# Kernel tuning notes

Measured on AMD Instinct MI355X. Metric: run time of the kernel, lower is better.

## Reference

```python
import jax, jax.numpy as jnp
import numpy as np

B, N, C, H, HD = 32, 512, 384, 6, 64
WH = WW = WT = 8
ALPHA = 4.0
KS = 5


def safe_pow(x, p):
    # x = relu(...) >= 0; avoid nan grads at x == 0
    pos = x > 0
    return jnp.where(pos, jnp.where(pos, x, 1.0) ** p, 0.0)


def setup_inputs() -> dict:
    key = jax.random.key(0)
    ks = jax.random.split(key, 12)
    s = 0.02
    return {
        "x": jax.random.normal(ks[0], (B, N, C), jnp.float32),
        "y": jax.random.normal(ks[1], (B, N, C), jnp.float32),
        "Wqkvg": jax.random.normal(ks[2], (4 * C, C), jnp.float32) * s,
        "bqkvg": jax.random.normal(ks[3], (4 * C,), jnp.float32) * s,
        "Wproj": jax.random.normal(ks[4], (C, C), jnp.float32) * s,
        "bproj": jax.random.normal(ks[5], (C,), jnp.float32) * s,
        "dwc_w": jax.random.normal(ks[6], (HD, 1, KS, KS, KS), jnp.float32) * s,
        "dwc_b": jax.random.normal(ks[7], (HD,), jnp.float32) * s,
        "power_p": jax.random.normal(ks[8], (1, H, 1, HD), jnp.float32) * s,
        "scale_p": jax.random.normal(ks[9], (1, 1, C), jnp.float32) * s,
        "pe": jax.random.normal(ks[10], (1, N, C), jnp.float32) * s,
    }


def reference(x, y, Wqkvg, bqkvg, Wproj, bproj, dwc_w, dwc_b, power_p, scale_p, pe):
    qkv = (x @ Wqkvg.T + bqkvg).reshape(B, N, 4, C)
    k = qkv[:, :, 1]
    v = qkv[:, :, 2]
    g = qkv[:, :, 3]
    q = (y @ Wqkvg.T + bqkvg).reshape(B, N, 4, C)[:, :, 0]

    k = k + pe
    scale = jax.nn.softplus(scale_p)          # (1,1,C)
    power = 1.0 + ALPHA * jax.nn.sigmoid(power_p)  # (1,H,1,HD)
    q = q / scale
    k = k / scale

    def heads(t):  # (B,N,C) -> (B,H,N,HD)
        return t.reshape(B, N, H, HD).transpose(0, 2, 1, 3)

    q = heads(q)
    k = heads(k)
    v = heads(v)

    q_pos = safe_pow(jax.nn.relu(q), power)
    q_neg = safe_pow(jax.nn.relu(-q), power)
    k_pos = safe_pow(jax.nn.relu(k), power)
    k_neg = safe_pow(jax.nn.relu(-k), power)

    q_sim = jnp.concatenate([q_pos, q_neg], axis=-1)   # (B,H,N,2HD)
    q_opp = jnp.concatenate([q_neg, q_pos], axis=-1)
    kf = jnp.concatenate([k_pos, k_neg], axis=-1)      # (B,H,N,2HD)
    v1, v2 = jnp.split(v, 2, axis=-1)                  # each (B,H,N,HD/2)

    k_mean = kf.mean(axis=-2)                          # (B,H,2HD)
    inv_sqrt_n = N ** (-0.5)
    kfs = kf * inv_sqrt_n

    z_sim = 1.0 / (jnp.einsum("bhnd,bhd->bhn", q_sim, k_mean)[..., None] + 1e-6)
    kv1 = jnp.einsum("bhnd,bhne->bhde", kfs, v1 * inv_sqrt_n)
    x_sim = jnp.einsum("bhnd,bhde->bhne", q_sim, kv1) * z_sim

    z_opp = 1.0 / (jnp.einsum("bhnd,bhd->bhn", q_opp, k_mean)[..., None] + 1e-6)
    kv2 = jnp.einsum("bhnd,bhne->bhde", kfs, v2 * inv_sqrt_n)
    x_opp = jnp.einsum("bhnd,bhde->bhne", q_opp, kv2) * z_opp

    xa = jnp.concatenate([x_sim, x_opp], axis=-1)      # (B,H,N,HD)
    xa = xa.transpose(0, 2, 1, 3).reshape(B, N, C)

    # depthwise conv3d on v: (B*H, HD, Wh, Ww, Wt)
    vr = v.reshape(B * H, WH, WW, WT, HD).transpose(0, 4, 1, 2, 3)
    pad = KS // 2
    vc = jax.lax.conv_general_dilated(
        vr, dwc_w, window_strides=(1, 1, 1),
        padding=[(pad, pad)] * 3,
        dimension_numbers=("NCDHW", "OIDHW", "NCDHW"),
        feature_group_count=HD,
    ) + dwc_b[None, :, None, None, None]
    vc = vc.transpose(0, 2, 3, 4, 1).reshape(B, N, C)

    out = (xa + vc) * g
    out = out @ Wproj.T + bproj
    return out
```

## Files before the change

### kernel.cpp

```cpp
#include <hip/hip_runtime.h>
#include <hip/hip_bf16.h>
#include <math.h>

#define B_  32
#define N_  512
#define C_  384
#define H_  6
#define HD_ 64
#define M_  (B_*N_)

typedef __attribute__((ext_vector_type(8))) short bfrag;
typedef __attribute__((ext_vector_type(8))) unsigned short u16x8;
typedef __attribute__((ext_vector_type(4))) float f32x4;

__device__ __forceinline__ unsigned short f2bfu(float f){
  unsigned int u = __float_as_uint(f);
  u += 0x7fffu + ((u >> 16) & 1u);
  return (unsigned short)(u >> 16);
}
__device__ __forceinline__ float bf2f(unsigned short u){
  return __uint_as_float(((unsigned int)u) << 16);
}
__device__ __forceinline__ bfrag cvt8(float4 a, float4 b){
  bfrag r;
  r[0]=(short)f2bfu(a.x); r[1]=(short)f2bfu(a.y); r[2]=(short)f2bfu(a.z); r[3]=(short)f2bfu(a.w);
  r[4]=(short)f2bfu(b.x); r[5]=(short)f2bfu(b.y); r[6]=(short)f2bfu(b.z); r[7]=(short)f2bfu(b.w);
  return r;
}
__device__ __forceinline__ void gload_lds16(const unsigned short* gp, unsigned short* lp){
  __builtin_amdgcn_global_load_lds(
      (const __attribute__((address_space(1))) void*)gp,
      (__attribute__((address_space(3))) void*)lp, 16, 0, 0);
}

__global__ void param_kernel(const float* __restrict__ scale_p,
                             const float* __restrict__ power_p,
                             float* __restrict__ scale_inv,
                             float* __restrict__ power){
  int t = threadIdx.x;
  if (t < C_){
    float s  = scale_p[t];
    scale_inv[t] = 1.0f / log1pf(expf(s));
  }
  if (t < H_*HD_){
    float p = power_p[t];
    power[t] = 1.0f + 4.0f / (1.0f + expf(-p));
  }
}

__global__ void sentinel_kernel(float* __restrict__ out, int n){
  int i = blockIdx.x*256 + threadIdx.x;
  if (i < n) out[i] = 1.0e9f;
}

__global__ __launch_bounds__(256) void cvt_bf16_kernel(
    const float* __restrict__ x, const float* __restrict__ y,
    const float* __restrict__ W, const float* __restrict__ Wp,
    unsigned short* __restrict__ xb, unsigned short* __restrict__ yb,
    unsigned short* __restrict__ Wb, unsigned short* __restrict__ Wpb)
{
  const int bid = blockIdx.x;
  const float* src; unsigned short* dst; int base;
  if (bid < 3072)      { src = x;  dst = xb;  base = bid; }
  else if (bid < 6144) { src = y;  dst = yb;  base = bid - 3072; }
  else if (bid < 6432) { src = W;  dst = Wb;  base = bid - 6144; }
  else                 { src = Wp; dst = Wpb; base = bid - 6432; }
  const size_t i0 = ((size_t)base*256 + threadIdx.x)*8;
  float4 a = *reinterpret_cast<const float4*>(src + i0);
  float4 b = *reinterpret_cast<const float4*>(src + i0 + 4);
  *reinterpret_cast<bfrag*>(dst + i0) = cvt8(a, b);
}

__global__ __launch_bounds__(256,4) void gemm_qkvg(
    const unsigned short* __restrict__ xb, const unsigned short* __restrict__ yb,
    const unsigned short* __restrict__ Wb, const float* __restrict__ bias,
    const float* __restrict__ pe, const float* __restrict__ scale_inv,
    const float* __restrict__ power,
    unsigned short* __restrict__ qf, unsigned short* __restrict__ kf,
    unsigned short* __restrict__ v, unsigned short* __restrict__ g)
{
  __shared__ unsigned short As[2][4096];
  __shared__ unsigned short Bs[2][4096];

  const int tid  = threadIdx.x;
  const int row0 = blockIdx.y * 128;
  const int col0 = blockIdx.x * 128;
  const int mode = blockIdx.x / 3;
  const unsigned short* Ab = (mode == 0) ? yb : xb;

  const int wave = tid >> 6, lane = tid & 63;
  const int wm = (wave >> 1) * 64, wn = (wave & 1) * 64;
  const int fr = lane & 15, quad = lane >> 4;
  const int srr = tid >> 2;
  const int skc = (tid & 3) * 8;

  const unsigned short* ga0 = &Ab[(size_t)(row0 + srr)*C_ + skc];
  const unsigned short* gb0 = &Wb[(size_t)(col0 + srr)*C_ + skc];
  const size_t gstep = (size_t)64*C_;

  f32x4 acc[4][4] = {};

  gload_lds16(ga0,         &As[0][tid*8]);
  gload_lds16(ga0 + gstep, &As[0][2048 + tid*8]);
  gload_lds16(gb0,         &Bs[0][tid*8]);
  gload_lds16(gb0 + gstep, &Bs[0][2048 + tid*8]);
  __syncthreads();

  #pragma unroll 2
  for (int t = 0; t < 12; t++){
    const int cur = t & 1;
    if (t < 11){
      const int k0 = (t+1)*32;
      gload_lds16(ga0 + k0,         &As[cur^1][tid*8]);
      gload_lds16(ga0 + gstep + k0, &As[cur^1][2048 + tid*8]);
      gload_lds16(gb0 + k0,         &Bs[cur^1][tid*8]);
      gload_lds16(gb0 + gstep + k0, &Bs[cur^1][2048 + tid*8]);
    }
    bfrag af[4], bf[4];
    #pragma unroll
    for (int f = 0; f < 4; f++){
      af[f] = *reinterpret_cast<const bfrag*>(&As[cur][(wm + f*16 + fr)*32 + quad*8]);
      bf[f] = *reinterpret_cast<const bfrag*>(&Bs[cur][(wn + f*16 + fr)*32 + quad*8]);
    }
    #pragma unroll
    for (int i=0;i<4;i++)
      #pragma unroll
      for (int j=0;j<4;j++)
        acc[i][j] = __builtin_amdgcn_mfma_f32_16x16x32_bf16(af[i], bf[j], acc[i][j], 0, 0, 0);
    __syncthreads();
  }

  const int cbase = col0 - mode*384;
  if (mode <= 1){
    unsigned short* dst = (mode == 0) ? qf : kf;
    #pragma unroll
    for (int i = 0; i < 4; i++){
      const int rowb = row0 + wm + i*16 + quad*4;
      #pragma unroll
      for (int j = 0; j < 4; j++){
        const int cc = cbase + wn + j*16 + fr;
        const int hh = cc >> 6, dd = cc & 63;
        const float bcol = bias[mode*384 + cc];
        const float scv  = scale_inv[cc];
        const float p    = power[cc];
        #pragma unroll
        for (int r = 0; r < 4; r++){
          const int row = rowb + r;
          float val = acc[i][j][r] + bcol;
          if (mode == 1) val += pe[(row & (N_-1))*C_ + cc];
          val *= scv;
          const float ax = fabsf(val);
          const float pv = (ax > 0.0f) ? exp2f(p * log2f(ax)) : 0.0f;
          const size_t o = (size_t)row*768 + hh*128 + dd;
          dst[o]      = f2bfu((val > 0.0f) ? pv : 0.0f);
          dst[o + 64] = f2bfu((val < 0.0f) ? pv : 0.0f);
        }
      }
    }
  } else {
    unsigned short* dst = (mode == 2) ? v : g;
    #pragma unroll
    for (int i = 0; i < 4; i++){
      const int rowb = row0 + wm + i*16 + quad*4;
      #pragma unroll
      for (int j = 0; j < 4; j++){
        const int cc = cbase + wn + j*16 + fr;
        const float bcol = bias[mode*384 + cc];
        #pragma unroll
        for (int r = 0; r < 4; r++)
          dst[(size_t)(rowb + r)*C_ + cc] = f2bfu(acc[i][j][r] + bcol);
      }
    }
  }
}

#define NC_ 256
__global__ __launch_bounds__(512) void attn_kernel(
    const unsigned short* __restrict__ qf, const unsigned short* __restrict__ kf,
    const unsigned short* __restrict__ v, float* __restrict__ xa)
{
  const int bh = blockIdx.x;
  const int b = bh / H_, h = bh % H_;
  __shared__ __align__(16) unsigned short smem[54912];
  unsigned short* kfT  = smem;
  unsigned short* vT   = smem + 33792;
  unsigned short* kvBT = smem;
  unsigned short* qs   = smem + 33792;

  const int tid = threadIdx.x;
  const int wave = tid >> 6, lane = tid & 63;
  const int fr = lane & 15, quad = lane >> 4;

  const unsigned short* kfg   = kf + (size_t)b*N_*768 + h*128;
  const unsigned short* vbase = v  + (size_t)b*N_*C_  + h*HD_;

  for (int i = tid; i < 16*NC_; i += 512){
    int e = 64 + (i >> 8);
    int nl = i & (NC_-1);
    vT[e*264 + nl] = (e == 64) ? (unsigned short)0x3F80 : (unsigned short)0;
  }
  __syncthreads();

  f32x4 acc[5] = {};
  for (int chunk = 0; chunk < 2; chunk++){
    const int n0 = chunk * NC_;
    for (int it = 0; it < 8; it++){
      int flat = it*512 + tid;
      int cg = flat & 15, nl = flat >> 4;
      u16x8 k8 = *reinterpret_cast<const u16x8*>(&kfg[(size_t)(n0+nl)*768 + cg*8]);
      #pragma unroll
      for (int j = 0; j < 8; j++) kfT[(cg*8+j)*264 + nl] = k8[j];
    }
    for (int it = 0; it < 4; it++){
      int flat = it*512 + tid;
      int cg = flat & 7, nl = flat >> 3;
      u16x8 v8 = *reinterpret_cast<const u16x8*>(&vbase[(size_t)(n0+nl)*C_ + cg*8]);
      #pragma unroll
      for (int j = 0; j < 8; j++) vT[(cg*8+j)*264 + nl] = v8[j];
    }
    __syncthreads();
    for (int kk = 0; kk < NC_/32; kk++){
      int ko = kk*32 + quad*8;
      bfrag af = *reinterpret_cast<const bfrag*>(&kfT[(wave*16 + fr)*264 + ko]);
      #pragma unroll
      for (int j = 0; j < 5; j++){
        bfrag bf = *reinterpret_cast<const bfrag*>(&vT[(j*16 + fr)*264 + ko]);
        acc[j] = __builtin_amdgcn_mfma_f32_16x16x32_bf16(af, bf, acc[j], 0, 0, 0);
      }
    }
    __syncthreads();
  }

  const float invN = 1.0f / (float)N_;
  {
    const int dbase = wave*16 + quad*4;
    #pragma unroll
    for (int j = 0; j < 4; j++){
      const int e = j*16 + fr;
      const int dd = (e < 32) ? dbase : (dbase ^ 64);
      ushort4 w4;
      w4.x = f2bfu(acc[j][0] * invN);
      w4.y = f2bfu(acc[j][1] * invN);
      w4.z = f2bfu(acc[j][2] * invN);
      w4.w = f2bfu(acc[j][3] * invN);
      *reinterpret_cast<ushort4*>(&kvBT[e*136 + dd]) = w4;
    }
    if (fr == 0){
      ushort4 wk;
      wk.x = f2bfu(acc[4][0] * invN);
      wk.y = f2bfu(acc[4][1] * invN);
      wk.z = f2bfu(acc[4][2] * invN);
      wk.w = f2bfu(acc[4][3] * invN);
      *reinterpret_cast<ushort4*>(&kvBT[64*136 + dbase]) = wk;
      *reinterpret_cast<ushort4*>(&kvBT[65*136 + (dbase^64)]) = wk;
    }
  }
  __syncthreads();

  const unsigned short* qfg = qf + (size_t)b*N_*768 + h*128;
  float* xabase = xa + (size_t)b*N_*C_ + h*HD_;
  for (int mc = 0; mc < 4; mc++){
    const int m0 = mc * 128;
    for (int it = 0; it < 4; it++){
      int flat = it*512 + tid;
      int cg = flat & 15, nl = flat >> 4;
      *reinterpret_cast<u16x8*>(&qs[nl*136 + cg*8]) =
          *reinterpret_cast<const u16x8*>(&qfg[(size_t)(m0+nl)*768 + cg*8]);
    }
    __syncthreads();
    f32x4 a2[5] = {};
    for (int kk = 0; kk < 4; kk++){
      int ko = kk*32 + quad*8;
      bfrag af = *reinterpret_cast<const bfrag*>(&qs[(wave*16 + fr)*136 + ko]);
      #pragma unroll
      for (int j = 0; j < 5; j++){
        bfrag bf = *reinterpret_cast<const bfrag*>(&kvBT[(j*16 + fr)*136 + ko]);
        a2[j] = __builtin_amdgcn_mfma_f32_16x16x32_bf16(af, bf, a2[j], 0, 0, 0);
      }
    }
    #pragma unroll
    for (int r = 0; r < 4; r++){
      const float zsim = __shfl(a2[4][r], quad*16);
      const float zopp = __shfl(a2[4][r], quad*16 + 1);
      const int n = m0 + wave*16 + quad*4 + r;
      #pragma unroll
      for (int j = 0; j < 4; j++){
        const int e = j*16 + fr;
        const float z = (e < 32) ? zsim : zopp;
        xabase[(size_t)n*C_ + e] = a2[j][r] / (z + 1e-6f);
      }
    }
    __syncthreads();
  }
}

__global__ __launch_bounds__(512) void conv_kernel(
    const unsigned short* __restrict__ v, const float* __restrict__ dwc_w,
    const float* __restrict__ dwc_b, const float* __restrict__ xa,
    const unsigned short* __restrict__ g, unsigned short* __restrict__ ab)
{
  const int bh = blockIdx.x;
  const int b = bh / H_, h = bh % H_;
  __shared__ float vol[32][521];
  __shared__ float wv[32][126];
  __shared__ float wb[32];
  const int tid = threadIdx.x;
  const unsigned short* vbase = v + (size_t)b*N_*C_ + h*HD_;
  const float* xabatch = xa + (size_t)b*N_*C_ + (size_t)h*N_*HD_;
  const unsigned short* gb = g + (size_t)b*N_*C_ + (size_t)h*N_*HD_;
  unsigned short* abb = ab + (size_t)b*N_*C_ + (size_t)h*N_*HD_;

  for (int half = 0; half < 2; half++){
    const int ch0 = half * 32;
    for (int it = 0; it < 32; it++){
      int flat = it*512 + tid;
      int cl = flat & 31, n = flat >> 5;
      vol[cl][n] = bf2f(vbase[(size_t)n*C_ + ch0 + cl]);
    }
    for (int i = tid; i < 32*125; i += 512){
      int ch = i / 125, wi = i - ch*125;
      wv[ch][wi] = dwc_w[(ch0+ch)*125 + wi];
    }
    if (tid < 32) wb[tid] = dwc_b[ch0 + tid];
    __syncthreads();

    for (int t = 0; t < 4; t++){
      const int task = t*512 + tid;
      const int ch = task & 31;
      const int zy = task >> 5;
      const int z = zy >> 3, yc = zy & 7;
      float o[8];
      const float bias = wb[ch];
      #pragma unroll
      for (int xx = 0; xx < 8; xx++) o[xx] = bias;
      #pragma unroll
      for (int kd = 0; kd < 5; kd++){
        const int zz = z + kd - 2;
        if ((unsigned)zz >= 8u) continue;
        #pragma unroll
        for (int kh = 0; kh < 5; kh++){
          const int yy = yc + kh - 2;
          if ((unsigned)yy >= 8u) continue;
          const float* row = &vol[ch][zz*64 + yy*8];
          float rr[8];
          #pragma unroll
          for (int xx = 0; xx < 8; xx++) rr[xx] = row[xx];
          const float* wrow = &wv[ch][kd*25 + kh*5];
          float w5[5];
          #pragma unroll
          for (int kw = 0; kw < 5; kw++) w5[kw] = wrow[kw];
          #pragma unroll
          for (int xx = 0; xx < 8; xx++){
            #pragma unroll
            for (int kw = 0; kw < 5; kw++){
              const int xi = xx + kw - 2;
              if ((unsigned)xi < 8u) o[xx] = fmaf(w5[kw], rr[xi], o[xx]);
            }
          }
        }
      }
      const int nb = zy * 8;
      #pragma unroll
      for (int xx = 0; xx < 8; xx++){
        const size_t di = (size_t)(nb + xx)*HD_ + ch0 + ch;
        abb[di] = f2bfu((xabatch[di] + o[xx]) * bf2f(gb[di]));
      }
    }
    __syncthreads();
  }
}

__global__ __launch_bounds__(256,4) void proj_kernel(
    const unsigned short* __restrict__ ab, const unsigned short* __restrict__ Wpb,
    const float* __restrict__ bp, float* __restrict__ out)
{
  __shared__ unsigned short As[2][4096];
  __shared__ unsigned short Bs[2][4096];

  const int tid  = threadIdx.x;
  const int row0 = blockIdx.y * 128;
  const int col0 = blockIdx.x * 128;
  const int wave = tid >> 6, lane = tid & 63;
  const int wm = (wave >> 1) * 64, wn = (wave & 1) * 64;
  const int fr = lane & 15, quad = lane >> 4;
  const int srr = tid >> 2;
  const int skc = (tid & 3) * 8;

  const unsigned short* ga0 = &ab[(size_t)(row0 + srr)*C_ + skc];
  const unsigned short* gb0 = &Wpb[(size_t)(col0 + srr)*C_ + skc];
  const size_t gstep = (size_t)64*C_;

  f32x4 acc[4][4] = {};

  gload_lds16(ga0,         &As[0][tid*8]);
  gload_lds16(ga0 + gstep, &As[0][2048 + tid*8]);
  gload_lds16(gb0,         &Bs[0][tid*8]);
  gload_lds16(gb0 + gstep, &Bs[0][2048 + tid*8]);
  __syncthreads();

  #pragma unroll 2
  for (int t = 0; t < 12; t++){
    const int cur = t & 1;
    if (t < 11){
      const int k0 = (t+1)*32;
      gload_lds16(ga0 + k0,         &As[cur^1][tid*8]);
      gload_lds16(ga0 + gstep + k0, &As[cur^1][2048 + tid*8]);
      gload_lds16(gb0 + k0,         &Bs[cur^1][tid*8]);
      gload_lds16(gb0 + gstep + k0, &Bs[cur^1][2048 + tid*8]);
    }
    bfrag af[4], bf[4];
    #pragma unroll
    for (int f = 0; f < 4; f++){
      af[f] = *reinterpret_cast<const bfrag*>(&As[cur][(wm + f*16 + fr)*32 + quad*8]);
      bf[f] = *reinterpret_cast<const bfrag*>(&Bs[cur][(wn + f*16 + fr)*32 + quad*8]);
    }
    #pragma unroll
    for (int i=0;i<4;i++)
      #pragma unroll
      for (int j=0;j<4;j++)
        acc[i][j] = __builtin_amdgcn_mfma_f32_16x16x32_bf16(af[i], bf[j], acc[i][j], 0, 0, 0);
    __syncthreads();
  }

  #pragma unroll
  for (int i = 0; i < 4; i++){
    const int rowb = row0 + wm + i*16 + quad*4;
    #pragma unroll
    for (int j = 0; j < 4; j++){
      const int col = col0 + wn + j*16 + fr;
      const float bcol = bp[col];
      #pragma unroll
      for (int r = 0; r < 4; r++)
        out[(size_t)(rowb + r)*C_ + col] = acc[i][j][r] + bcol;
    }
  }
}

extern "C" void kernel_launch(void* const* d_in, const int* in_sizes, int n_in,
                              void* d_out, int out_size, void* d_ws, size_t ws_size,
                              hipStream_t stream){
  float* out = (float*)d_out;

  const int expect[11] = {6291456, 6291456, 589824, 1536, 147456, 384, 8000, 64, 384, 384, 196608};
  bool ok = (n_in == 11);
  for (int i = 0; ok && i < 11; i++) ok = (in_sizes[i] == expect[i]);
  if (!ok){
    sentinel_kernel<<<(out_size+255)/256, 256, 0, stream>>>(out, out_size);
    return;
  }

  const float* x    = (const float*)d_in[0];
  const float* y    = (const float*)d_in[1];
  const float* W    = (const float*)d_in[2];
  const float* bq   = (const float*)d_in[3];
  const float* Wp   = (const float*)d_in[4];
  const float* bp   = (const float*)d_in[5];
  const float* dwcw = (const float*)d_in[6];
  const float* dwcb = (const float*)d_in[7];
  const float* pwp  = (const float*)d_in[8];
  const float* scp  = (const float*)d_in[9];
  const float* pe   = (const float*)d_in[10];

  float* ws = (float*)d_ws;
  const size_t SZ = (size_t)M_ * C_;
  unsigned short* qf  = (unsigned short*)ws;
  unsigned short* kfb = qf + 2*SZ;
  unsigned short* v   = (unsigned short*)(ws + 2*SZ);
  unsigned short* g   = v + SZ;
  unsigned short* xb  = (unsigned short*)(ws + 3*SZ);
  unsigned short* yb  = xb + SZ;
  float* xa = ws + 3*SZ;
  unsigned short* ab  = (unsigned short*)ws;
  unsigned short* Wb  = (unsigned short*)(ws + 4*SZ);
  unsigned short* Wpb = Wb + 589824;
  float* scale_inv = (float*)(Wpb + 147456);
  float* power     = scale_inv + 512;

  param_kernel<<<1, 512, 0, stream>>>(scp, pwp, scale_inv, power);
  cvt_bf16_kernel<<<6504, 256, 0, stream>>>(x, y, W, Wp, xb, yb, Wb, Wpb);
  gemm_qkvg<<<dim3(12, 128), 256, 0, stream>>>(xb, yb, Wb, bq, pe, scale_inv, power, qf, kfb, v, g);
  attn_kernel<<<dim3(B_*H_), 512, 0, stream>>>(qf, kfb, v, xa);
  conv_kernel<<<dim3(B_*H_), 512, 0, stream>>>(v, dwcw, dwcb, xa, g, ab);
  proj_kernel<<<dim3(3, 128), 256, 0, stream>>>(ab, Wpb, bp, out);
}
```

Measured before the change: 267.5 us.

## Stage q/k feature epilogue through LDS, swizzle attn transposes, split conv channels

The QKVG GEMM epilogue for q/k features now writes each 64-row half into a swizzled shared-memory tile, then stores it to global memory as coalesced 16-byte vectors instead of scattered 2-byte stores. The attention kernel's transposed kf/v LDS tiles get an XOR swizzle meant to reduce bank conflicts on the scalar transpose writes. The conv kernel is split across four channel groups per (batch, head) to raise parallelism, and two launch-bounds occupancy hints are dropped. The extra syncs in the epilogue and the larger conv grid add some overhead in exchange.

```diff
diff --git a/kernel.cpp b/kernel.cpp
--- a/kernel.cpp
+++ b/kernel.cpp
@@ -71,7 +71,7 @@
   *reinterpret_cast<bfrag*>(dst + i0) = cvt8(a, b);
 }
 
-__global__ __launch_bounds__(256,4) void gemm_qkvg(
+__global__ __launch_bounds__(256) void gemm_qkvg(
     const unsigned short* __restrict__ xb, const unsigned short* __restrict__ yb,
     const unsigned short* __restrict__ Wb, const float* __restrict__ bias,
     const float* __restrict__ pe, const float* __restrict__ scale_inv,
@@ -79,8 +79,7 @@
     unsigned short* __restrict__ qf, unsigned short* __restrict__ kf,
     unsigned short* __restrict__ v, unsigned short* __restrict__ g)
 {
-  __shared__ unsigned short As[2][4096];
-  __shared__ unsigned short Bs[2][4096];
+  __shared__ __align__(16) unsigned short smem[16384];
 
   const int tid  = threadIdx.x;
   const int row0 = blockIdx.y * 128;
@@ -100,10 +99,10 @@
 
   f32x4 acc[4][4] = {};
 
-  gload_lds16(ga0,         &As[0][tid*8]);
-  gload_lds16(ga0 + gstep, &As[0][2048 + tid*8]);
-  gload_lds16(gb0,         &Bs[0][tid*8]);
-  gload_lds16(gb0 + gstep, &Bs[0][2048 + tid*8]);
+  gload_lds16(ga0,         &smem[tid*8]);
+  gload_lds16(ga0 + gstep, &smem[2048 + tid*8]);
+  gload_lds16(gb0,         &smem[8192 + tid*8]);
+  gload_lds16(gb0 + gstep, &smem[8192 + 2048 + tid*8]);
   __syncthreads();
 
   #pragma unroll 2
@@ -111,16 +110,17 @@
     const int cur = t & 1;
     if (t < 11){
       const int k0 = (t+1)*32;
-      gload_lds16(ga0 + k0,         &As[cur^1][tid*8]);
-      gload_lds16(ga0 + gstep + k0, &As[cur^1][2048 + tid*8]);
-      gload_lds16(gb0 + k0,         &Bs[cur^1][tid*8]);
-      gload_lds16(gb0 + gstep + k0, &Bs[cur^1][2048 + tid*8]);
+      const int nxt = cur^1;
+      gload_lds16(ga0 + k0,         &smem[nxt*4096 + tid*8]);
+      gload_lds16(ga0 + gstep + k0, &smem[nxt*4096 + 2048 + tid*8]);
+      gload_lds16(gb0 + k0,         &smem[8192 + nxt*4096 + tid*8]);
+      gload_lds16(gb0 + gstep + k0, &smem[8192 + nxt*4096 + 2048 + tid*8]);
     }
     bfrag af[4], bf[4];
     #pragma unroll
     for (int f = 0; f < 4; f++){
-      af[f] = *reinterpret_cast<const bfrag*>(&As[cur][(wm + f*16 + fr)*32 + quad*8]);
-      bf[f] = *reinterpret_cast<const bfrag*>(&Bs[cur][(wn + f*16 + fr)*32 + quad*8]);
+      af[f] = *reinterpret_cast<const bfrag*>(&smem[cur*4096 + (wm + f*16 + fr)*32 + quad*8]);
+      bf[f] = *reinterpret_cast<const bfrag*>(&smem[8192 + cur*4096 + (wn + f*16 + fr)*32 + quad*8]);
     }
     #pragma unroll
     for (int i=0;i<4;i++)
@@ -133,29 +133,46 @@
   const int cbase = col0 - mode*384;
   if (mode <= 1){
     unsigned short* dst = (mode == 0) ? qf : kf;
-    #pragma unroll
-    for (int i = 0; i < 4; i++){
-      const int rowb = row0 + wm + i*16 + quad*4;
-      #pragma unroll
-      for (int j = 0; j < 4; j++){
-        const int cc = cbase + wn + j*16 + fr;
-        const int hh = cc >> 6, dd = cc & 63;
-        const float bcol = bias[mode*384 + cc];
-        const float scv  = scale_inv[cc];
-        const float p    = power[cc];
+    const int hh0 = cbase >> 6;
+    for (int pass = 0; pass < 2; pass++){
+      if ((wave >> 1) == pass){
+        const int swz = quad << 3;
         #pragma unroll
-        for (int r = 0; r < 4; r++){
-          const int row = rowb + r;
-          float val = acc[i][j][r] + bcol;
-          if (mode == 1) val += pe[(row & (N_-1))*C_ + cc];
-          val *= scv;
-          const float ax = fabsf(val);
-          const float pv = (ax > 0.0f) ? exp2f(p * log2f(ax)) : 0.0f;
-          const size_t o = (size_t)row*768 + hh*128 + dd;
-          dst[o]      = f2bfu((val > 0.0f) ? pv : 0.0f);
-          dst[o + 64] = f2bfu((val < 0.0f) ? pv : 0.0f);
+        for (int i = 0; i < 4; i++){
+          const int rloc = i*16 + quad*4;
+          #pragma unroll
+          for (int j = 0; j < 4; j++){
+            const int cl = wn + j*16 + fr;
+            const int hl = cl >> 6, dd = cl & 63;
+            const int cc = cbase + cl;
+            const float bcol = bias[mode*384 + cc];
+            const float scv  = scale_inv[cc];
+            const float p    = power[cc];
+            const int fpos = (hl*128 + dd) ^ swz;
+            #pragma unroll
+            for (int r = 0; r < 4; r++){
+              const int row = row0 + pass*64 + rloc + r;
+              float val = acc[i][j][r] + bcol;
+              if (mode == 1) val += pe[(row & (N_-1))*C_ + cc];
+              val *= scv;
+              const float ax = fabsf(val);
+              const float pv = (ax > 0.0f) ? exp2f(p * log2f(ax)) : 0.0f;
+              smem[(rloc + r)*256 + fpos]      = f2bfu((val > 0.0f) ? pv : 0.0f);
+              smem[(rloc + r)*256 + fpos + 64] = f2bfu((val < 0.0f) ? pv : 0.0f);
+            }
+          }
         }
       }
+      __syncthreads();
+      #pragma unroll
+      for (int it = 0; it < 8; it++){
+        const int idx = it*256 + tid;
+        const int rl = idx >> 5, cb = idx & 31;
+        const int bswz = (rl >> 2) & 3;
+        u16x8 val = *reinterpret_cast<const u16x8*>(&smem[rl*256 + ((cb ^ bswz) << 3)]);
+        *reinterpret_cast<u16x8*>(&dst[(size_t)(row0 + pass*64 + rl)*768 + hh0*128 + cb*8]) = val;
+      }
+      __syncthreads();
     }
   } else {
     unsigned short* dst = (mode == 2) ? v : g;
@@ -207,25 +224,31 @@
     for (int it = 0; it < 8; it++){
       int flat = it*512 + tid;
       int cg = flat & 15, nl = flat >> 4;
+      int swz = cg << 3;
       u16x8 k8 = *reinterpret_cast<const u16x8*>(&kfg[(size_t)(n0+nl)*768 + cg*8]);
       #pragma unroll
-      for (int j = 0; j < 8; j++) kfT[(cg*8+j)*264 + nl] = k8[j];
+      for (int j = 0; j < 8; j++) kfT[(cg*8+j)*264 + (nl ^ swz)] = k8[j];
     }
     for (int it = 0; it < 4; it++){
       int flat = it*512 + tid;
       int cg = flat & 7, nl = flat >> 3;
+      int swz = cg << 3;
       u16x8 v8 = *reinterpret_cast<const u16x8*>(&vbase[(size_t)(n0+nl)*C_ + cg*8]);
       #pragma unroll
-      for (int j = 0; j < 8; j++) vT[(cg*8+j)*264 + nl] = v8[j];
+      for (int j = 0; j < 8; j++) vT[(cg*8+j)*264 + (nl ^ swz)] = v8[j];
     }
     __syncthreads();
+    const int arow = wave*16 + fr;
+    const int aswz = (arow >> 3) << 3;
     for (int kk = 0; kk < NC_/32; kk++){
       int ko = kk*32 + quad*8;
-      bfrag af = *reinterpret_cast<const bfrag*>(&kfT[(wave*16 + fr)*264 + ko]);
+      bfrag af = *reinterpret_cast<const bfrag*>(&kfT[arow*264 + (ko ^ aswz)]);
       #pragma unroll
       for (int j = 0; j < 5; j++){
-        bfrag bf = *reinterpret_cast<const bfrag*>(&vT[(j*16 + fr)*264 + ko]);
-        acc[j] = __builtin_amdgcn_mfma_f32_16x16x32_bf16(af, bf, acc[j], 0, 0, 0);
+        const int brow = j*16 + fr;
+        const int bswz = (brow >> 3) << 3;
+        bfrag bfr = *reinterpret_cast<const bfrag*>(&vT[brow*264 + (ko ^ bswz)]);
+        acc[j] = __builtin_amdgcn_mfma_f32_16x16x32_bf16(af, bfr, acc[j], 0, 0, 0);
       }
     }
     __syncthreads();
@@ -274,8 +297,8 @@
       bfrag af = *reinterpret_cast<const bfrag*>(&qs[(wave*16 + fr)*136 + ko]);
       #pragma unroll
       for (int j = 0; j < 5; j++){
-        bfrag bf = *reinterpret_cast<const bfrag*>(&kvBT[(j*16 + fr)*136 + ko]);
-        a2[j] = __builtin_amdgcn_mfma_f32_16x16x32_bf16(af, bf, a2[j], 0, 0, 0);
+        bfrag bfr = *reinterpret_cast<const bfrag*>(&kvBT[(j*16 + fr)*136 + ko]);
+        a2[j] = __builtin_amdgcn_mfma_f32_16x16x32_bf16(af, bfr, a2[j], 0, 0, 0);
       }
     }
     #pragma unroll
@@ -301,76 +324,73 @@
 {
   const int bh = blockIdx.x;
   const int b = bh / H_, h = bh % H_;
-  __shared__ float vol[32][521];
-  __shared__ float wv[32][126];
-  __shared__ float wb[32];
+  const int ch0 = blockIdx.y * 16;
+  __shared__ float vol[16][521];
+  __shared__ float wv[16][126];
+  __shared__ float wb[16];
   const int tid = threadIdx.x;
   const unsigned short* vbase = v + (size_t)b*N_*C_ + h*HD_;
   const float* xabatch = xa + (size_t)b*N_*C_ + (size_t)h*N_*HD_;
   const unsigned short* gb = g + (size_t)b*N_*C_ + (size_t)h*N_*HD_;
   unsigned short* abb = ab + (size_t)b*N_*C_ + (size_t)h*N_*HD_;
 
-  for (int half = 0; half < 2; half++){
-    const int ch0 = half * 32;
-    for (int it = 0; it < 32; it++){
-      int flat = it*512 + tid;
-      int cl = flat & 31, n = flat >> 5;
-      vol[cl][n] = bf2f(vbase[(size_t)n*C_ + ch0 + cl]);
-    }
-    for (int i = tid; i < 32*125; i += 512){
-      int ch = i / 125, wi = i - ch*125;
-      wv[ch][wi] = dwc_w[(ch0+ch)*125 + wi];
-    }
-    if (tid < 32) wb[tid] = dwc_b[ch0 + tid];
-    __syncthreads();
-
-    for (int t = 0; t < 4; t++){
-      const int task = t*512 + tid;
-      const int ch = task & 31;
-      const int zy = task >> 5;
-      const int z = zy >> 3, yc = zy & 7;
-      float o[8];
-      const float bias = wb[ch];
-      #pragma unroll
-      for (int xx = 0; xx < 8; xx++) o[xx] = bias;
-      #pragma unroll
-      for (int kd = 0; kd < 5; kd++){
-        const int zz = z + kd - 2;
-        if ((unsigned)zz >= 8u) continue;
+  for (int it = 0; it < 16; it++){
+    int flat = it*512 + tid;
+    int cl = flat & 15, n = flat >> 4;
+    vol[cl][n] = bf2f(vbase[(size_t)n*C_ + ch0 + cl]);
+  }
+  for (int i = tid; i < 16*125; i += 512){
+    int ch = i / 125, wi = i - ch*125;
+    wv[ch][wi] = dwc_w[(ch0+ch)*125 + wi];
+  }
+  if (tid < 16) wb[tid] = dwc_b[ch0 + tid];
+  __syncthreads();
+
+  for (int t = 0; t < 2; t++){
+    const int task = t*512 + tid;
+    const int ch = task & 15;
+    const int zy = task >> 4;
+    const int z = zy >> 3, yc = zy & 7;
+    float o[8];
+    const float bias = wb[ch];
+    #pragma unroll
+    for (int xx = 0; xx < 8; xx++) o[xx] = bias;
+    #pragma unroll
+    for (int kd = 0; kd < 5; kd++){
+      const int zz = z + kd - 2;
+      if ((unsigned)zz >= 8u) continue;
+      #pragma unroll
+      for (int kh = 0; kh < 5; kh++){
+        const int yy = yc + kh - 2;
+        if ((unsigned)yy >= 8u) continue;
+        const float* row = &vol[ch][zz*64 + yy*8];
+        float rr[8];
         #pragma unroll
-        for (int kh = 0; kh < 5; kh++){
-          const int yy = yc + kh - 2;
-          if ((unsigned)yy >= 8u) continue;
-          const float* row = &vol[ch][zz*64 + yy*8];
-          float rr[8];
+        for (int xx = 0; xx < 8; xx++) rr[xx] = row[xx];
+        const float* wrow = &wv[ch][kd*25 + kh*5];
+        float w5[5];
+        #pragma unroll
+        for (int kw = 0; kw < 5; kw++) w5[kw] = wrow[kw];
+        #pragma unroll
+        for (int xx = 0; xx < 8; xx++){
           #pragma unroll
-          for (int xx = 0; xx < 8; xx++) rr[xx] = row[xx];
-          const float* wrow = &wv[ch][kd*25 + kh*5];
-          float w5[5];
-          #pragma unroll
-          for (int kw = 0; kw < 5; kw++) w5[kw] = wrow[kw];
-          #pragma unroll
-          for (int xx = 0; xx < 8; xx++){
-            #pragma unroll
-            for (int kw = 0; kw < 5; kw++){
-              const int xi = xx + kw - 2;
-              if ((unsigned)xi < 8u) o[xx] = fmaf(w5[kw], rr[xi], o[xx]);
-            }
+          for (int kw = 0; kw < 5; kw++){
+            const int xi = xx + kw - 2;
+            if ((unsigned)xi < 8u) o[xx] = fmaf(w5[kw], rr[xi], o[xx]);
           }
         }
       }
-      const int nb = zy * 8;
-      #pragma unroll
-      for (int xx = 0; xx < 8; xx++){
-        const size_t di = (size_t)(nb + xx)*HD_ + ch0 + ch;
-        abb[di] = f2bfu((xabatch[di] + o[xx]) * bf2f(gb[di]));
-      }
-    }
-    __syncthreads();
-  }
-}
-
-__global__ __launch_bounds__(256,4) void proj_kernel(
+    }
+    const int nb = zy * 8;
+    #pragma unroll
+    for (int xx = 0; xx < 8; xx++){
+      const size_t di = (size_t)(nb + xx)*HD_ + ch0 + ch;
+      abb[di] = f2bfu((xabatch[di] + o[xx]) * bf2f(gb[di]));
+    }
+  }
+}
+
+__global__ __launch_bounds__(256) void proj_kernel(
     const unsigned short* __restrict__ ab, const unsigned short* __restrict__ Wpb,
     const float* __restrict__ bp, float* __restrict__ out)
 {
@@ -480,6 +500,6 @@
   cvt_bf16_kernel<<<6504, 256, 0, stream>>>(x, y, W, Wp, xb, yb, Wb, Wpb);
   gemm_qkvg<<<dim3(12, 128), 256, 0, stream>>>(xb, yb, Wb, bq, pe, scale_inv, power, qf, kfb, v, g);
   attn_kernel<<<dim3(B_*H_), 512, 0, stream>>>(qf, kfb, v, xa);
-  conv_kernel<<<dim3(B_*H_), 512, 0, stream>>>(v, dwcw, dwcb, xa, g, ab);
+  conv_kernel<<<dim3(B_*H_, 4), 512, 0, stream>>>(v, dwcw, dwcb, xa, g, ab);
   proj_kernel<<<dim3(3, 128), 256, 0, stream>>>(ab, Wpb, bp, out);
 }
```

Result: slower. 314.2 us (+17.4%).
